# Kernel optimization log

Hardware: AMD Instinct MI355X
Metric: run time of the kernel (lower is better)

## Reference

```python
import jax, jax.numpy as jnp
import numpy as np

_T = lambda a: jnp.swapaxes(a, -1, -2)
EPS_TRI = 0.01   # block_tridiagonal_solve epsilon
EPS_CHOL = 0.01  # block_cholesky epsilon
EPS_BS = 1e-4    # batch_block_cholesky_solve epsilon


def _forward(z_samples, A_base, b_base, Q_sqrt, ms, Ri_sqrts, noise):
    n, T, K = z_samples.shape
    D = A_base.shape[-1]
    I = jnp.eye(D, dtype=z_samples.dtype)

    # ---- AQbFunction on z_samples[:, :-1]
    zt = z_samples[:, :-1]                                    # [n,T-1,K]
    As = jnp.einsum('ntk,kij->ntij', zt, A_base)              # [n,T-1,D,D]
    bs = jnp.einsum('ntk,kd->ntd', zt, b_base)                # [n,T-1,D]
    Qi_sqrts = jnp.einsum('ntk,kij->ntij', zt, Q_sqrt)        # [n,T-1,D,D]

    # ---- convert_lds_to_block_tridiag
    Qis = Qi_sqrts @ _T(Qi_sqrts)                             # [n,T-1,D,D]
    Ris = Ri_sqrts @ _T(Ri_sqrts)                             # [T,D,D]
    Jl = -jnp.einsum('ntij,ntjk->ntik', Qis, As)              # [n,T-1,D,D]
    pad_t = lambda a, w: jnp.pad(a, ((0, 0), w) + ((0, 0),) * (a.ndim - 2))
    Jd = (pad_t(-jnp.einsum('ntji,ntjk->ntik', As, Jl), (0, 1))
          + pad_t(Qis, (1, 0)) + Ris[None])                   # [n,T,D,D]
    h = (pad_t(jnp.einsum('ntij,ntj->nti', Jl, bs), (0, 1))
         + pad_t(jnp.einsum('ntij,ntj->nti', Qis, bs), (1, 0))
         + jnp.einsum('tij,tj->ti', Ris, ms)[None])           # [n,T,D]

    # time-major for scans
    Jd_t = jnp.swapaxes(Jd, 0, 1)    # [T,n,D,D]
    Jl_t = jnp.swapaxes(Jl, 0, 1)    # [T-1,n,D,D]
    h_t = jnp.swapaxes(h, 0, 1)      # [T,n,D]

    # ---- block_tridiagonal_solve (Thomas-style forward elim + back subst)
    J0 = Jd_t[0] + EPS_TRI * I
    c0 = _T(jnp.linalg.solve(J0, _T(Jl_t[0])))
    d0 = jnp.linalg.solve(J0, h_t[0][..., None])[..., 0]
    Jl_pad = jnp.concatenate([Jl_t, jnp.zeros_like(Jl_t[:1])], 0)  # [T,n,D,D]

    def fwd_step(carry, x):
        c_prev, d_prev = carry
        Jd_k, Jl_prev, Jl_cur, h_k = x
        Jk = Jd_k - Jl_prev @ c_prev + EPS_TRI * I
        c_k = _T(jnp.linalg.solve(Jk, _T(Jl_cur)))
        rhs = h_k - (Jl_prev @ d_prev[..., None])[..., 0]
        d_k = jnp.linalg.solve(Jk, rhs[..., None])[..., 0]
        return (c_k, d_k), (c_k, d_k)

    _, (cs, ds) = jax.lax.scan(fwd_step, (c0, d0),
                               (Jd_t[1:], Jl_t, Jl_pad[1:], h_t[1:]))
    d_all = jnp.concatenate([d0[None], ds], 0)   # [T,n,D]
    c_all = jnp.concatenate([c0[None], cs[:-1]], 0)  # [T-1,n,D,D]

    def bwd_step(x_next, inp):
        d_k, c_k = inp
        x_k = d_k - (c_k @ x_next[..., None])[..., 0]
        return x_k, x_k

    _, xs = jax.lax.scan(bwd_step, d_all[-1], (d_all[:-1], c_all), reverse=True)
    mu = jnp.swapaxes(jnp.concatenate([xs, d_all[-1:]], 0), 0, 1)  # [n,T,D]

    # ---- block_cholesky
    L0 = jnp.linalg.cholesky(Jd_t[0] + EPS_CHOL * I)

    def chol_step(L_prev, x):
        Jd_k, Jl_k = x
        Ll = _T(jnp.linalg.solve(_T(L_prev), _T(Jl_k)))
        L_k = jnp.linalg.cholesky(Jd_k - Ll @ _T(Ll) + EPS_CHOL * I)
        return L_k, (L_k, Ll)

    _, (Ls, Lls) = jax.lax.scan(chol_step, L0, (Jd_t[1:], Jl_t))
    L_all = jnp.concatenate([L0[None], Ls], 0)   # [T,n,D,D]

    # ---- batch_block_cholesky_solve (forward substitution on regularized L^T)
    Lr = L_all + EPS_BS * I
    z_t = jnp.swapaxes(noise.reshape(n, T, D), 0, 1)  # [T,n,D]
    x0 = jnp.linalg.solve(_T(Lr[0]), z_t[0][..., None])[..., 0]

    def samp_step(x_prev, inp):
        L_k, Ll_prev, zk = inp
        rhs = zk - (_T(Ll_prev) @ x_prev[..., None])[..., 0]
        x_k = jnp.linalg.solve(_T(L_k), rhs[..., None])[..., 0]
        return x_k, x_k

    _, xs2 = jax.lax.scan(samp_step, x0, (Lr[1:], Lls, z_t[1:]))
    x = jnp.swapaxes(jnp.concatenate([x0[None], xs2], 0), 0, 1)  # [n,T,D]
    return x + mu


def setup_inputs() -> dict:
    key = jax.random.key(0)
    k = jax.random.split(key, 7)
    n, T, D, K = 64, 256, 32, 8
    dt = jnp.float32
    I = jnp.eye(D, dtype=dt)
    z_samples = jax.random.normal(k[0], (n, T, K), dt)
    noise = jax.random.normal(k[1], (n, T * D), dt)
    # params per LDSVariational/AQbFunction init (+ tiny jitter to avoid degeneracy)
    A_base = 0.8 * jnp.tile(I, (K, 1, 1)) + 0.01 * jax.random.normal(k[2], (K, D, D), dt)
    b_base = 0.01 * jax.random.normal(k[3], (K, D), dt)
    Q_sqrt = jnp.tile(I, (K, 1, 1)) + 0.01 * jax.random.normal(k[4], (K, D, D), dt)
    ms = 0.1 * jax.random.normal(k[5], (T, D), dt)
    Ri_sqrts = 10.0 * jnp.tile(I, (T, 1, 1)) + 0.01 * jax.random.normal(k[6], (T, D, D), dt)  # 1/sqrt(0.01)=10
    return {"z_samples": z_samples, "A_base": A_base, "b_base": b_base,
            "Q_sqrt": Q_sqrt, "ms": ms, "Ri_sqrts": Ri_sqrts, "noise": noise}


def reference(z_samples, A_base, b_base, Q_sqrt, ms, Ri_sqrts, noise):
    return _forward(z_samples, A_base, b_base, Q_sqrt, ms, Ri_sqrts, noise)
```

## Files before the change

### kernel.cpp

```cpp
#include <hip/hip_runtime.h>
#include <cstddef>

#define LD 33
#define IDX(r,c) ((r)*LD+(c))
#define EPS_TRI 0.01f
#define EPS_BS 1e-4f
#define F4C(v,e) ((e)==0?(v).x:(e)==1?(v).y:(e)==2?(v).z:(v).w)
#define WAVE_FENCE() __builtin_amdgcn_wave_barrier()

#define NCH0 14
#define CSZ0 19
#define NCH1 18
#define CSZ1 15
#define WARM 6


__device__ __forceinline__ float4 xor1(const float4 v) {
  float4 r;
  r.x = __shfl_xor(v.x, 1);
  r.y = __shfl_xor(v.y, 1);
  r.z = __shfl_xor(v.z, 1);
  r.w = __shfl_xor(v.w, 1);
  return r;
}

__global__ __launch_bounds__(256) void ris_kernel(const float* __restrict__ Ri,
                                                  const float* __restrict__ ms,
                                                  float* __restrict__ Ris,
                                                  float* __restrict__ Rm) {
  const int t = blockIdx.x;
  const int tid = threadIdx.x;
  __shared__ float sR[32*LD];
  __shared__ float sRis[32*LD];
  __shared__ float sm[32];
  {
    const int e = tid * 4;
    const int r = e >> 5, c = e & 31;
    const float4 v = *(const float4*)(Ri + (size_t)t*1024 + e);
    sR[IDX(r,c)+0] = v.x; sR[IDX(r,c)+1] = v.y; sR[IDX(r,c)+2] = v.z; sR[IDX(r,c)+3] = v.w;
    if (tid < 32) sm[tid] = ms[t*32 + tid];
  }
  __syncthreads();
  const int r = tid >> 3, c0 = (tid & 7) * 4;
  float a0=0.f,a1=0.f,a2=0.f,a3=0.f;
#pragma unroll
  for (int p = 0; p < 32; p++) {
    const float rr = sR[IDX(r,p)];
    a0 += rr * sR[IDX(c0+0,p)];
    a1 += rr * sR[IDX(c0+1,p)];
    a2 += rr * sR[IDX(c0+2,p)];
    a3 += rr * sR[IDX(c0+3,p)];
  }
  sRis[IDX(r,c0+0)] = a0; sRis[IDX(r,c0+1)] = a1;
  sRis[IDX(r,c0+2)] = a2; sRis[IDX(r,c0+3)] = a3;
  float4 o; o.x=a0; o.y=a1; o.z=a2; o.w=a3;
  *(float4*)(Ris + (size_t)t*1024 + r*32 + c0) = o;
  __syncthreads();
  if (tid < 32) {
    float acc = 0.f;
#pragma unroll
    for (int j = 0; j < 32; j++) acc += sRis[IDX(tid,j)] * sm[j];
    Rm[t*32 + tid] = acc;
  }
}

__global__ __launch_bounds__(256) void pre_kernel(
    const float* __restrict__ z, const float* __restrict__ A_base,
    const float* __restrict__ b_base, const float* __restrict__ Q_sqrt,
    const float* __restrict__ Ris, const float* __restrict__ Rm,
    float* __restrict__ Jdb, float* __restrict__ Pm, float* __restrict__ h_ws) {
  const int n = blockIdx.x >> 8;
  const int t = blockIdx.x & 255;
  const int tid = threadIdx.x;
  const int r = tid >> 3, c0 = (tid & 7) * 4;
  const bool hcv = (t < 255);
  const bool hpv = (t >= 1);
  __shared__ __align__(16) float sAs[32*LD], sQs[32*LD], sQsp[32*LD];
  __shared__ __align__(16) float sQis[32*LD], sQisp[32*LD], sP[32*LD];
  __shared__ float s_z[16];
  __shared__ float s_bs[32], s_bsp[32];
  if (tid < 8)       s_z[tid] = hcv ? z[((size_t)n << 11) + t*8 + tid] : 0.f;
  else if (tid < 16) s_z[tid] = hpv ? z[((size_t)n << 11) + (t-1)*8 + (tid-8)] : 0.f;
  __syncthreads();
  {
    float a0=0,a1=0,a2=0,a3=0,q0=0,q1=0,q2=0,q3=0,p0=0,p1=0,p2=0,p3=0;
#pragma unroll
    for (int kq = 0; kq < 8; kq++) {
      const float zc = s_z[kq], zp = s_z[8+kq];
      const float4 av = *(const float4*)(A_base + kq*1024 + r*32 + c0);
      const float4 qv = *(const float4*)(Q_sqrt + kq*1024 + r*32 + c0);
      a0 += zc*av.x; a1 += zc*av.y; a2 += zc*av.z; a3 += zc*av.w;
      q0 += zc*qv.x; q1 += zc*qv.y; q2 += zc*qv.z; q3 += zc*qv.w;
      p0 += zp*qv.x; p1 += zp*qv.y; p2 += zp*qv.z; p3 += zp*qv.w;
    }
    sAs[IDX(r,c0+0)]=a0; sAs[IDX(r,c0+1)]=a1; sAs[IDX(r,c0+2)]=a2; sAs[IDX(r,c0+3)]=a3;
    sQs[IDX(r,c0+0)]=q0; sQs[IDX(r,c0+1)]=q1; sQs[IDX(r,c0+2)]=q2; sQs[IDX(r,c0+3)]=q3;
    sQsp[IDX(r,c0+0)]=p0; sQsp[IDX(r,c0+1)]=p1; sQsp[IDX(r,c0+2)]=p2; sQsp[IDX(r,c0+3)]=p3;
    if (tid < 32) {
      float b = 0.f;
#pragma unroll
      for (int kq = 0; kq < 8; kq++) b += s_z[kq] * b_base[kq*32 + tid];
      s_bs[tid] = b;
    } else if (tid < 64) {
      const int i = tid - 32;
      float b = 0.f;
#pragma unroll
      for (int kq = 0; kq < 8; kq++) b += s_z[8+kq] * b_base[kq*32 + i];
      s_bsp[i] = b;
    }
  }
  __syncthreads();
  {
    float a0=0,a1=0,a2=0,a3=0,b0=0,b1=0,b2=0,b3=0;
#pragma unroll
    for (int p = 0; p < 32; p++) {
      const float qr = sQs[IDX(r,p)];
      a0 += qr * sQs[IDX(c0+0,p)];
      a1 += qr * sQs[IDX(c0+1,p)];
      a2 += qr * sQs[IDX(c0+2,p)];
      a3 += qr * sQs[IDX(c0+3,p)];
      const float pr2 = sQsp[IDX(r,p)];
      b0 += pr2 * sQsp[IDX(c0+0,p)];
      b1 += pr2 * sQsp[IDX(c0+1,p)];
      b2 += pr2 * sQsp[IDX(c0+2,p)];
      b3 += pr2 * sQsp[IDX(c0+3,p)];
    }
    sQis[IDX(r,c0+0)]=a0; sQis[IDX(r,c0+1)]=a1; sQis[IDX(r,c0+2)]=a2; sQis[IDX(r,c0+3)]=a3;
    sQisp[IDX(r,c0+0)]=b0; sQisp[IDX(r,c0+1)]=b1; sQisp[IDX(r,c0+2)]=b2; sQisp[IDX(r,c0+3)]=b3;
  }
  __syncthreads();
  {
    float a0=0,a1=0,a2=0,a3=0;
#pragma unroll
    for (int p = 0; p < 32; p++) {
      const float qr = sQis[IDX(r,p)];
      a0 += qr * sAs[IDX(p,c0+0)];
      a1 += qr * sAs[IDX(p,c0+1)];
      a2 += qr * sAs[IDX(p,c0+2)];
      a3 += qr * sAs[IDX(p,c0+3)];
    }
    sP[IDX(r,c0+0)]=a0; sP[IDX(r,c0+1)]=a1; sP[IDX(r,c0+2)]=a2; sP[IDX(r,c0+3)]=a3;
    if (hcv) {
      float4 v; v.x=a0; v.y=a1; v.z=a2; v.w=a3;
      *(float4*)(Pm + ((size_t)(n*255 + t))*1024 + r*32 + c0) = v;
    }
  }
  __syncthreads();
  {
    const float4 rv = *(const float4*)(Ris + (size_t)t*1024 + r*32 + c0);
    float j0 = rv.x, j1 = rv.y, j2 = rv.z, j3 = rv.w;
    if (r == c0+0) j0 += EPS_TRI;
    else if (r == c0+1) j1 += EPS_TRI;
    else if (r == c0+2) j2 += EPS_TRI;
    else if (r == c0+3) j3 += EPS_TRI;
    if (hcv) {
#pragma unroll
      for (int p = 0; p < 32; p++) {
        const float ar = sAs[IDX(p,r)];
        j0 += ar * sP[IDX(p,c0+0)];
        j1 += ar * sP[IDX(p,c0+1)];
        j2 += ar * sP[IDX(p,c0+2)];
        j3 += ar * sP[IDX(p,c0+3)];
      }
    }
    if (hpv) {
      j0 += sQisp[IDX(r,c0+0)];
      j1 += sQisp[IDX(r,c0+1)];
      j2 += sQisp[IDX(r,c0+2)];
      j3 += sQisp[IDX(r,c0+3)];
    }
    float4 v; v.x=j0; v.y=j1; v.z=j2; v.w=j3;
    *(float4*)(Jdb + ((size_t)(n*256 + t))*1024 + r*32 + c0) = v;
    if (tid < 32) {
      float h = Rm[t*32 + tid];
      if (hcv) {
        float a = 0.f;
#pragma unroll
        for (int j = 0; j < 32; j++) a += sP[IDX(tid,j)] * s_bs[j];
        h -= a;
      }
      if (hpv) {
        float a = 0.f;
#pragma unroll
        for (int j = 0; j < 32; j++) a += sQisp[IDX(tid,j)] * s_bsp[j];
        h += a;
      }
      h_ws[((size_t)(n*256 + t))*32 + tid] = h;
    }
  }
}

union __align__(16) ChainShared {
  struct {
    float sCT[32*36];
    float sB[32*36];
    float sPiv[64];
    float s_rhs[32], s_d[32], s_invp[32];
  } r0;
  struct {
    float sLl[32*36];
    float sLT[32*36];
    float sLrow[32*36];
    float sCol[32];
    float s_x[32], s_invd[32], s_invr[32];
  } r1;
};

__global__ __launch_bounds__(64) void chain_kernel(
    const float* __restrict__ Jdb, const float* __restrict__ Pm,
    const float* __restrict__ h_ws, const float* __restrict__ noise,
    float* __restrict__ c_ws, float* __restrict__ d_ws, float* __restrict__ x_ws) {
  const int bid  = blockIdx.x;
  const int role = (bid >= 64*NCH0) ? 1 : 0;
  const int rem  = bid - role*64*NCH0;
  const int bn   = rem & 63;
  const int ch   = rem >> 6;
  const int lane = threadIdx.x;
  const int r    = lane >> 1;
  const int h2   = lane & 1;
  const int c16  = h2 * 16;

  const int csz       = role ? CSZ1 : CSZ0;
  const int k_out     = ch * csz;
  const int k_start   = (ch == 0) ? 0 : (k_out - WARM);
  const int k_end_raw = k_out + csz;
  const int k_end     = (k_end_raw > 256) ? 256 : k_end_raw;

  const float* Jb = Jdb + (size_t)bn * 256 * 1024;
  const float* Pb = Pm  + (size_t)bn * 255 * 1024;

  __shared__ ChainShared su;

  if (role == 0) {
    float* sCT = su.r0.sCT;
    float* sB  = su.r0.sB;
    float* sPiv = su.r0.sPiv;
    float* s_rhs = su.r0.s_rhs;
    float* s_d   = su.r0.s_d;
    float* s_invp = su.r0.s_invp;
    const float* hb = h_ws + (size_t)bn * 256 * 32;

    const int offO = c16;
    const int offX = 16 - c16;

    float jrow[16]; float4 pq[4]; float hq;
    {
      float4 j4[4];
#pragma unroll
      for (int q = 0; q < 4; q++) j4[q] = *(const float4*)(Jb + (size_t)k_start*1024 + r*32 + c16 + 4*q);
#pragma unroll
      for (int q = 0; q < 4; q++) pq[q] = *(const float4*)(Pb + (size_t)k_start*1024 + r*32 + c16 + 4*q);
      hq = hb[k_start*32 + r];
#pragma unroll
      for (int i = 0; i < 16; i++) jrow[i] = F4C(j4[i >> 2], i & 3);
    }

    for (int k = k_start; k < k_end; k++) {
      float4 jn4[4], pn[4]; float hn = 0.f;
      if (k + 1 < 256) {
#pragma unroll
        for (int q = 0; q < 4; q++)
          jn4[q] = *(const float4*)(Jb + (size_t)(k+1)*1024 + r*32 + c16 + 4*q);
        hn = hb[(k+1)*32 + r];
        if (k + 1 < 255) {
#pragma unroll
          for (int q = 0; q < 4; q++)
            pn[q] = *(const float4*)(Pb + (size_t)(k+1)*1024 + r*32 + c16 + 4*q);
        }
      }
      if (h2 == 0) s_rhs[r] = hq;
      float g[32];
      if (h2 == 1) {
#pragma unroll
        for (int i = 0; i < 32; i++) g[i] = (i == r) ? 1.f : 0.f;
      }
#pragma unroll
      for (int i = 0; i < 16; i++) {
        const float oth = __shfl_xor(jrow[i], 1);
        if (h2 == 0) { g[i] = jrow[i]; g[16+i] = oth; }
      }
      if (r == 0) {
#pragma unroll
        for (int q = 0; q < 8; q++) {
          float4 v; v.x=g[4*q]; v.y=g[4*q+1]; v.z=g[4*q+2]; v.w=g[4*q+3];
          *(float4*)(&sPiv[h2*32 + 4*q]) = v;
        }
      }
      WAVE_FENCE();
      float my_piv = 1.f;
#pragma unroll
      for (int j = 0; j < 32; j++) {
        const float pj_own = sPiv[h2*32 + j];
        const float pj_oth = __shfl_xor(pj_own, 1);
        const float dpiv = h2 ? pj_oth : pj_own;
        const float ip = __builtin_amdgcn_rcpf(dpiv);
        const float gj_own = g[j];
        const float gj_oth = __shfl_xor(gj_own, 1);
        float f = (h2 ? gj_oth : gj_own) * ip;
        if (j == r) { my_piv = dpiv; f = 0.f; }
#pragma unroll
        for (int q = 0; q < 8; q++) {
          const float4 v = *(const float4*)(&sPiv[h2*32 + 4*q]);
          g[4*q+0] -= f * v.x;
          g[4*q+1] -= f * v.y;
          g[4*q+2] -= f * v.z;
          g[4*q+3] -= f * v.w;
        }
        if (j + 1 < 32) {
          WAVE_FENCE();
          if (r == j + 1) {
#pragma unroll
            for (int q = 0; q < 8; q++) {
              float4 v; v.x=g[4*q]; v.y=g[4*q+1]; v.z=g[4*q+2]; v.w=g[4*q+3];
              *(float4*)(&sPiv[h2*32 + 4*q]) = v;
            }
          }
          WAVE_FENCE();
        }
      }
      const float ipv = __builtin_amdgcn_rcpf(my_piv);
      if (h2 == 0) s_invp[r] = ipv;
      else {
        const int s7 = r & 7;
#pragma unroll
        for (int q = 0; q < 8; q++) {
          float4 v; v.x=g[4*q]; v.y=g[4*q+1]; v.z=g[4*q+2]; v.w=g[4*q+3];
          *(float4*)(&sB[r*36 + 4*(q ^ s7)]) = v;
        }
      }
      WAVE_FENCE();
      if (h2 == 1) {
        float acc = 0.f;
#pragma unroll
        for (int q = 0; q < 8; q++) {
          const float4 rv = *(const float4*)(&s_rhs[4*q]);
          acc += g[4*q]*rv.x + g[4*q+1]*rv.y + g[4*q+2]*rv.z + g[4*q+3]*rv.w;
        }
        const float dv = acc * ipv;
        s_d[r] = dv;
        if (k >= k_out) d_ws[((size_t)(bn*256 + k))*32 + r] = dv;
      }
      float4 poK[4];
      if (k < 255) {
#pragma unroll
        for (int q = 0; q < 4; q++) poK[q] = xor1(pq[q]);
        float outv[16];
#pragma unroll
        for (int i = 0; i < 16; i++) {
          const int c = c16 + i;
          const float* bb = &sB[c*36];
          const int s7 = c & 7;
          float acc = 0.f;
#pragma unroll
          for (int q = 0; q < 4; q++) {
            const float4 v0 = *(const float4*)(bb + 4*((4*h2 + q) ^ s7));
            acc += pq[q].x*v0.x + pq[q].y*v0.y + pq[q].z*v0.z + pq[q].w*v0.w;
            const float4 v1 = *(const float4*)(bb + 4*(((4 - 4*h2) + q) ^ s7));
            acc += poK[q].x*v1.x + poK[q].y*v1.y + poK[q].z*v1.z + poK[q].w*v1.w;
          }
          outv[i] = -acc * s_invp[c];
        }
        if (k >= k_out) {
#pragma unroll
          for (int q = 0; q < 4; q++) {
            float4 v; v.x=outv[4*q]; v.y=outv[4*q+1]; v.z=outv[4*q+2]; v.w=outv[4*q+3];
            *(float4*)(c_ws + ((size_t)(bn*255 + k))*1024 + r*32 + c16 + 4*q) = v;
          }
        }
#pragma unroll
        for (int i = 0; i < 16; i++) sCT[(c16+i)*36 + r] = outv[i];
      }
      WAVE_FENCE();
      if (k + 1 < k_end) {
        float a_own = 0.f;
#pragma unroll
        for (int q = 0; q < 4; q++) {
          const float4 dv = *(const float4*)(&s_d[c16 + 4*q]);
          a_own += pq[q].x*dv.x + pq[q].y*dv.y + pq[q].z*dv.z + pq[q].w*dv.w;
        }
        hq = hn + a_own + __shfl_xor(a_own, 1);
#pragma unroll
        for (int i = 0; i < 16; i++) {
          const float* base = &sCT[(c16 + i) * 36];
          float acc = F4C(jn4[i >> 2], i & 3);
#pragma unroll
          for (int q = 0; q < 4; q++) {
            const float4 v0 = *(const float4*)(base + offO + 4*q);
            acc += pq[q].x*v0.x + pq[q].y*v0.y + pq[q].z*v0.z + pq[q].w*v0.w;
            const float4 v1 = *(const float4*)(base + offX + 4*q);
            acc += poK[q].x*v1.x + poK[q].y*v1.y + poK[q].z*v1.z + poK[q].w*v1.w;
          }
          jrow[i] = acc;
        }
#pragma unroll
        for (int q = 0; q < 4; q++) pq[q] = pn[q];
      }
    }
  } else {
    float* sLl   = su.r1.sLl;
    float* sLT   = su.r1.sLT;
    float* sLrow = su.r1.sLrow;
    float* sCol  = su.r1.sCol;
    float* s_x   = su.r1.s_x;
    float* s_invd = su.r1.s_invd;
    float* s_invr = su.r1.s_invr;
    const float* nb = noise + (size_t)bn * 8192;

    float mrow[16]; float4 pq[4]; float xr;
    {
      float4 j4[4];
#pragma unroll
      for (int q = 0; q < 4; q++) j4[q] = *(const float4*)(Jb + (size_t)k_start*1024 + r*32 + c16 + 4*q);
#pragma unroll
      for (int q = 0; q < 4; q++) pq[q] = *(const float4*)(Pb + (size_t)k_start*1024 + r*32 + c16 + 4*q);
      xr = nb[k_start*32 + r];
#pragma unroll
      for (int i = 0; i < 16; i++) mrow[i] = F4C(j4[i >> 2], i & 3);
    }

    for (int k = k_start; k < k_end; k++) {
      float4 jn4[4], pn[4]; float nn = 0.f;
      if (k + 1 < 256) {
#pragma unroll
        for (int q = 0; q < 4; q++)
          jn4[q] = *(const float4*)(Jb + (size_t)(k+1)*1024 + r*32 + c16 + 4*q);
        nn = nb[(k+1)*32 + r];
        if (k + 1 < 255) {
#pragma unroll
          for (int q = 0; q < 4; q++)
            pn[q] = *(const float4*)(Pb + (size_t)(k+1)*1024 + r*32 + c16 + 4*q);
        }
      }
#pragma unroll
      for (int j = 0; j < 32; j++) {
        const int jl = j & 15, jh = j >> 4;
        WAVE_FENCE();
        if (h2 == jh) sCol[r] = mrow[jl];
        WAVE_FENCE();
        const float dpiv = sCol[j];
        const float fr   = sCol[r];
        const float sq = sqrtf(dpiv);
        const float inv = __builtin_amdgcn_rcpf(sq);
        if (h2 == 0 && r >= j) {
          const float lv = (r == j) ? sq : fr*inv;
          sLT[36*j + 4*((r>>2) ^ (j&7)) + (r&3)] = lv;
          sLrow[36*r + 4*((j>>2) ^ (r&7)) + (j&3)] = lv;
        }
        if (lane == 0) { s_invd[j] = inv; s_invr[j] = __builtin_amdgcn_rcpf(sq + EPS_BS); }
        const float s2 = (r > j) ? fr*inv*inv : 0.f;
#pragma unroll
        for (int q = 0; q < 4; q++) {
          const float4 cc = *(const float4*)(&sCol[c16 + 4*q]);
          mrow[4*q+0] -= s2 * cc.x;
          mrow[4*q+1] -= s2 * cc.y;
          mrow[4*q+2] -= s2 * cc.z;
          mrow[4*q+3] -= s2 * cc.w;
        }
      }
      WAVE_FENCE();
      float sv[16];
      if (k < 255) {
#pragma unroll
        for (int q = 0; q < 4; q++) {
          sv[4*q+0] = -pq[q].x; sv[4*q+1] = -pq[q].y;
          sv[4*q+2] = -pq[q].z; sv[4*q+3] = -pq[q].w;
        }
#pragma unroll
        for (int j = 31; j >= 0; j--) {
          const int jl = j & 15, jh = j >> 4;
          const float invdj = s_invd[j];
          const float v = sv[jl] * invdj;
          const float w = __shfl_xor(v, 1);
          const float xj = (h2 == jh) ? v : w;
          if (h2 == jh) sv[jl] = v;
#pragma unroll
          for (int q = 0; q < 4; q++) {
            if (4*q < j) {
              const float4 lv = *(const float4*)(&sLrow[36*j + 4*(((h2<<2)+q) ^ (j&7))]);
#pragma unroll
              for (int e = 0; e < 4; e++) {
                const int iLo = 4*q+e, iHi = 16+4*q+e;
                const float le = F4C(lv, e);
                if (iHi < j) {
                  sv[4*q+e] -= le * xj;
                } else if (iLo < j) {
                  const float m = (h2 == 0) ? le : 0.f;
                  sv[4*q+e] -= m * xj;
                }
              }
            }
          }
        }
        const int s7r = r & 7;
#pragma unroll
        for (int q = 0; q < 4; q++) {
          float4 v4; v4.x=sv[4*q]; v4.y=sv[4*q+1]; v4.z=sv[4*q+2]; v4.w=sv[4*q+3];
          *(float4*)(&sLl[36*r + 4*(((h2<<2)+q) ^ s7r)]) = v4;
        }
      }
      WAVE_FENCE();
      if (k + 1 < k_end) {
        float lrow[32];
#pragma unroll
        for (int gi = 0; gi < 16; gi++) {
          const float o = __shfl_xor(sv[gi], 1);
          lrow[gi]      = h2 ? o : sv[gi];
          lrow[16 + gi] = h2 ? sv[gi] : o;
        }
#pragma unroll
        for (int i = 0; i < 16; i++) {
          const int c = c16 + i;
          const int s7c = c & 7;
          float acc = 0.f;
#pragma unroll
          for (int q = 0; q < 8; q++) {
            const float4 v4 = *(const float4*)(&sLl[36*c + 4*(q ^ s7c)]);
            acc += lrow[4*q]*v4.x + lrow[4*q+1]*v4.y + lrow[4*q+2]*v4.z + lrow[4*q+3]*v4.w;
          }
          mrow[i] = F4C(jn4[i >> 2], i & 3) - acc;
        }
      }
      {
        float lc[32];
        const int s7r = r & 7;
#pragma unroll
        for (int q = 0; q < 8; q++) {
          const float4 v = *(const float4*)(&sLT[36*r + 4*(q ^ s7r)]);
          lc[4*q]=v.x; lc[4*q+1]=v.y; lc[4*q+2]=v.z; lc[4*q+3]=v.w;
        }
        float xp = xr;
        float myx = 0.f;
#pragma unroll
        for (int j = 31; j >= 0; j--) {
          const float xj = __shfl(xp * s_invr[j], 2*j);
          if (j == r) myx = xj;
          if (r < j) xp -= lc[j] * xj;
        }
        if (h2 == 0) {
          s_x[r] = myx;
          if (k >= k_out) x_ws[((size_t)(bn*256 + k))*32 + r] = myx;
        }
      }
      WAVE_FENCE();
      if (k + 1 < k_end) {
        float a_own = 0.f;
        const int rg = r >> 2, re = r & 3;
#pragma unroll
        for (int jj = 0; jj < 16; jj++)
          a_own += sLl[36*(c16+jj) + 4*(rg ^ (jj & 7)) + re] * s_x[c16+jj];
        xr = nn - (a_own + __shfl_xor(a_own, 1));
#pragma unroll
        for (int q = 0; q < 4; q++) pq[q] = pn[q];
      }
    }
  }
}

__global__ __launch_bounds__(64) void bwd_kernel(const float* __restrict__ c_ws,
                                                 const float* __restrict__ d_ws,
                                                 const float* __restrict__ x_ws,
                                                 float* __restrict__ out) {
  const int bn = blockIdx.x >> 4;
  const int q  = blockIdx.x & 15;
  const int lane = threadIdx.x;
  const int r = lane >> 1, h2 = lane & 1, c16 = h2 * 16;
  const int k_lo = q * 16;
  const int k_seed = (q == 15) ? 255 : (k_lo + 23);
  __shared__ float s_mu[32];
  if (h2 == 0) {
    const float mu = d_ws[((size_t)(bn*256 + k_seed))*32 + r];
    s_mu[r] = mu;
    if (k_seed == 255)
      out[((size_t)(bn*256 + 255))*32 + r] = x_ws[((size_t)(bn*256 + 255))*32 + r] + mu;
  }
  WAVE_FENCE();
  for (int k = k_seed - 1; k >= k_lo; k--) {
    const float* cp = c_ws + ((size_t)(bn*255 + k))*1024 + r*32 + c16;
    const float4 v0 = *(const float4*)(cp + 0);
    const float4 v1 = *(const float4*)(cp + 4);
    const float4 v2 = *(const float4*)(cp + 8);
    const float4 v3 = *(const float4*)(cp + 12);
    float part = v0.x*s_mu[c16+0] + v0.y*s_mu[c16+1] + v0.z*s_mu[c16+2] + v0.w*s_mu[c16+3]
               + v1.x*s_mu[c16+4] + v1.y*s_mu[c16+5] + v1.z*s_mu[c16+6] + v1.w*s_mu[c16+7]
               + v2.x*s_mu[c16+8] + v2.y*s_mu[c16+9] + v2.z*s_mu[c16+10]+ v2.w*s_mu[c16+11]
               + v3.x*s_mu[c16+12]+ v3.y*s_mu[c16+13]+ v3.z*s_mu[c16+14]+ v3.w*s_mu[c16+15];
    part += __shfl_xor(part, 1);
    float mu = 0.f, xv = 0.f;
    if (h2 == 0) {
      mu = d_ws[((size_t)(bn*256 + k))*32 + r] - part;
      xv = x_ws[((size_t)(bn*256 + k))*32 + r];
    }
    WAVE_FENCE();
    if (h2 == 0) {
      s_mu[r] = mu;
      if (k < k_lo + 16) out[((size_t)(bn*256 + k))*32 + r] = xv + mu;
    }
    WAVE_FENCE();
  }
}

extern "C" void kernel_launch(void* const* d_in, const int* in_sizes, int n_in,
                              void* d_out, int out_size, void* d_ws, size_t ws_size,
                              hipStream_t stream) {
  const float* z      = (const float*)d_in[0];
  const float* A_base = (const float*)d_in[1];
  const float* b_base = (const float*)d_in[2];
  const float* Q_sqrt = (const float*)d_in[3];
  const float* ms     = (const float*)d_in[4];
  const float* Ri     = (const float*)d_in[5];
  const float* noise  = (const float*)d_in[6];
  float* out = (float*)d_out;

  float* ws = (float*)d_ws;
  const size_t SZ_C = (size_t)64*255*1024;
  const size_t SZ_J = (size_t)64*256*1024;
  const size_t SZ_V = (size_t)64*256*32;

  float* c_ws  = ws;
  float* Jdb   = c_ws + SZ_C;
  float* Pm    = Jdb + SZ_J;
  float* hbuf  = Pm + SZ_C;
  float* d_vec = hbuf + SZ_V;
  float* x_vec = d_vec + SZ_V;
  float* Ris   = x_vec + SZ_V;
  float* Rm    = Ris + (size_t)256*1024;

  ris_kernel<<<256, 256, 0, stream>>>(Ri, ms, Ris, Rm);
  pre_kernel<<<16384, 256, 0, stream>>>(z, A_base, b_base, Q_sqrt, Ris, Rm, Jdb, Pm, hbuf);
  chain_kernel<<<64*(NCH0+NCH1), 64, 0, stream>>>(Jdb, Pm, hbuf, noise, c_ws, d_vec, x_vec);
  bwd_kernel<<<1024, 64, 0, stream>>>(c_ws, d_vec, x_vec, out);
}
```

Measured before the change: 1.029 ms.

## Split chain kernel into separate solve and Cholesky kernels with finer chunks

Replaces the single role-dispatched chain kernel with two kernels, one for the block-tridiagonal forward elimination and one for the Cholesky sampling chain. Each kernel uses 32 chunks of 8 steps with a 6-step warm-up, so more independent blocks run at once and the sequential chain per block is shorter. The elimination loop is also restructured: the Schur update and the rhs update now happen at the top of each step, and the XOR-swizzled shared layouts are replaced by plain rows. In exchange, the warm-up steps are a larger share of total work, there is an extra launch, and the two roles no longer overlap within one grid.

```diff
diff --git a/kernel.cpp b/kernel.cpp
--- a/kernel.cpp
+++ b/kernel.cpp
@@ -8,12 +8,9 @@
 #define F4C(v,e) ((e)==0?(v).x:(e)==1?(v).y:(e)==2?(v).z:(v).w)
 #define WAVE_FENCE() __builtin_amdgcn_wave_barrier()
 
-#define NCH0 14
-#define CSZ0 19
-#define NCH1 18
-#define CSZ1 15
+#define NCH 32
+#define CSZ 8
 #define WARM 6
-
 
 __device__ __forceinline__ float4 xor1(const float4 v) {
   float4 r;
@@ -190,368 +187,383 @@
   }
 }
 
-union __align__(16) ChainShared {
-  struct {
-    float sCT[32*36];
-    float sB[32*36];
-    float sPiv[64];
-    float s_rhs[32], s_d[32], s_invp[32];
-  } r0;
-  struct {
-    float sLl[32*36];
-    float sLT[32*36];
-    float sLrow[32*36];
-    float sCol[32];
-    float s_x[32], s_invd[32], s_invr[32];
-  } r1;
-};
-
-__global__ __launch_bounds__(64) void chain_kernel(
+__global__ __launch_bounds__(64) void chain0_kernel(
     const float* __restrict__ Jdb, const float* __restrict__ Pm,
-    const float* __restrict__ h_ws, const float* __restrict__ noise,
-    float* __restrict__ c_ws, float* __restrict__ d_ws, float* __restrict__ x_ws) {
-  const int bid  = blockIdx.x;
-  const int role = (bid >= 64*NCH0) ? 1 : 0;
-  const int rem  = bid - role*64*NCH0;
-  const int bn   = rem & 63;
-  const int ch   = rem >> 6;
+    const float* __restrict__ h_ws,
+    float* __restrict__ c_ws, float* __restrict__ d_ws) {
+  const int bn   = blockIdx.x & 63;
+  const int ch   = blockIdx.x >> 6;
   const int lane = threadIdx.x;
   const int r    = lane >> 1;
   const int h2   = lane & 1;
   const int c16  = h2 * 16;
 
-  const int csz       = role ? CSZ1 : CSZ0;
-  const int k_out     = ch * csz;
+  const int k_out     = ch * CSZ;
   const int k_start   = (ch == 0) ? 0 : (k_out - WARM);
-  const int k_end_raw = k_out + csz;
+  const int k_end_raw = k_out + CSZ;
   const int k_end     = (k_end_raw > 256) ? 256 : k_end_raw;
+  const int vec_start = k_start;
 
   const float* Jb = Jdb + (size_t)bn * 256 * 1024;
   const float* Pb = Pm  + (size_t)bn * 255 * 1024;
-
-  __shared__ ChainShared su;
-
-  if (role == 0) {
-    float* sCT = su.r0.sCT;
-    float* sB  = su.r0.sB;
-    float* sPiv = su.r0.sPiv;
-    float* s_rhs = su.r0.s_rhs;
-    float* s_d   = su.r0.s_d;
-    float* s_invp = su.r0.s_invp;
-    const float* hb = h_ws + (size_t)bn * 256 * 32;
-
-    const int offO = c16;
-    const int offX = 16 - c16;
-
-    float jrow[16]; float4 pq[4]; float hq;
+  const float* hb = h_ws + (size_t)bn * 256 * 32;
+
+  __shared__ float sCT[32*36];
+  __shared__ float sB[32*36];
+  __shared__ float sPiv[64];
+  __shared__ float s_rhs[32], s_d[32], s_invp[32];
+
+  float4 jq[4], pq[4], pq_prev[4]; float hq;
+#pragma unroll
+  for (int q = 0; q < 4; q++) jq[q] = *(const float4*)(Jb + (size_t)k_start*1024 + r*32 + c16 + 4*q);
+#pragma unroll
+  for (int q = 0; q < 4; q++) pq[q] = *(const float4*)(Pb + (size_t)k_start*1024 + r*32 + c16 + 4*q);
+#pragma unroll
+  for (int q = 0; q < 4; q++) pq_prev[q] = pq[q];
+  hq = hb[k_start*32 + r];
+
+  for (int k = k_start; k < k_end; k++) {
+    float4 jn[4], pn[4]; float hn = 0.f;
+    if (k + 1 < 256) {
+#pragma unroll
+      for (int q = 0; q < 4; q++)
+        jn[q] = *(const float4*)(Jb + (size_t)(k+1)*1024 + r*32 + c16 + 4*q);
+      hn = hb[(k+1)*32 + r];
+      if (k + 1 < 255) {
+#pragma unroll
+        for (int q = 0; q < 4; q++)
+          pn[q] = *(const float4*)(Pb + (size_t)(k+1)*1024 + r*32 + c16 + 4*q);
+      }
+    }
+    float prA[16], prB[16];
     {
-      float4 j4[4];
-#pragma unroll
-      for (int q = 0; q < 4; q++) j4[q] = *(const float4*)(Jb + (size_t)k_start*1024 + r*32 + c16 + 4*q);
-#pragma unroll
-      for (int q = 0; q < 4; q++) pq[q] = *(const float4*)(Pb + (size_t)k_start*1024 + r*32 + c16 + 4*q);
-      hq = hb[k_start*32 + r];
-#pragma unroll
-      for (int i = 0; i < 16; i++) jrow[i] = F4C(j4[i >> 2], i & 3);
-    }
-
-    for (int k = k_start; k < k_end; k++) {
-      float4 jn4[4], pn[4]; float hn = 0.f;
-      if (k + 1 < 256) {
-#pragma unroll
-        for (int q = 0; q < 4; q++)
-          jn4[q] = *(const float4*)(Jb + (size_t)(k+1)*1024 + r*32 + c16 + 4*q);
-        hn = hb[(k+1)*32 + r];
-        if (k + 1 < 255) {
-#pragma unroll
-          for (int q = 0; q < 4; q++)
-            pn[q] = *(const float4*)(Pb + (size_t)(k+1)*1024 + r*32 + c16 + 4*q);
-        }
-      }
-      if (h2 == 0) s_rhs[r] = hq;
-      float g[32];
-      if (h2 == 1) {
-#pragma unroll
-        for (int i = 0; i < 32; i++) g[i] = (i == r) ? 1.f : 0.f;
-      }
+      float own[16], oth[16];
+#pragma unroll
+      for (int i = 0; i < 16; i++) own[i] = F4C(pq_prev[i >> 2], i & 3);
+#pragma unroll
+      for (int i = 0; i < 16; i++) oth[i] = __shfl_xor(own[i], 1);
 #pragma unroll
       for (int i = 0; i < 16; i++) {
-        const float oth = __shfl_xor(jrow[i], 1);
-        if (h2 == 0) { g[i] = jrow[i]; g[16+i] = oth; }
-      }
-      if (r == 0) {
-#pragma unroll
-        for (int q = 0; q < 8; q++) {
-          float4 v; v.x=g[4*q]; v.y=g[4*q+1]; v.z=g[4*q+2]; v.w=g[4*q+3];
-          *(float4*)(&sPiv[h2*32 + 4*q]) = v;
-        }
-      }
-      WAVE_FENCE();
-      float my_piv = 1.f;
-#pragma unroll
-      for (int j = 0; j < 32; j++) {
-        const float pj_own = sPiv[h2*32 + j];
-        const float pj_oth = __shfl_xor(pj_own, 1);
-        const float dpiv = h2 ? pj_oth : pj_own;
-        const float ip = __builtin_amdgcn_rcpf(dpiv);
-        const float gj_own = g[j];
-        const float gj_oth = __shfl_xor(gj_own, 1);
-        float f = (h2 ? gj_oth : gj_own) * ip;
-        if (j == r) { my_piv = dpiv; f = 0.f; }
-#pragma unroll
-        for (int q = 0; q < 8; q++) {
-          const float4 v = *(const float4*)(&sPiv[h2*32 + 4*q]);
-          g[4*q+0] -= f * v.x;
-          g[4*q+1] -= f * v.y;
-          g[4*q+2] -= f * v.z;
-          g[4*q+3] -= f * v.w;
-        }
-        if (j + 1 < 32) {
-          WAVE_FENCE();
-          if (r == j + 1) {
-#pragma unroll
-            for (int q = 0; q < 8; q++) {
-              float4 v; v.x=g[4*q]; v.y=g[4*q+1]; v.z=g[4*q+2]; v.w=g[4*q+3];
-              *(float4*)(&sPiv[h2*32 + 4*q]) = v;
-            }
-          }
-          WAVE_FENCE();
-        }
-      }
-      const float ipv = __builtin_amdgcn_rcpf(my_piv);
-      if (h2 == 0) s_invp[r] = ipv;
-      else {
-        const int s7 = r & 7;
-#pragma unroll
-        for (int q = 0; q < 8; q++) {
-          float4 v; v.x=g[4*q]; v.y=g[4*q+1]; v.z=g[4*q+2]; v.w=g[4*q+3];
-          *(float4*)(&sB[r*36 + 4*(q ^ s7)]) = v;
-        }
-      }
-      WAVE_FENCE();
-      if (h2 == 1) {
-        float acc = 0.f;
-#pragma unroll
-        for (int q = 0; q < 8; q++) {
-          const float4 rv = *(const float4*)(&s_rhs[4*q]);
-          acc += g[4*q]*rv.x + g[4*q+1]*rv.y + g[4*q+2]*rv.z + g[4*q+3]*rv.w;
-        }
-        const float dv = acc * ipv;
-        s_d[r] = dv;
-        if (k >= k_out) d_ws[((size_t)(bn*256 + k))*32 + r] = dv;
-      }
-      float4 poK[4];
-      if (k < 255) {
-#pragma unroll
-        for (int q = 0; q < 4; q++) poK[q] = xor1(pq[q]);
-        float outv[16];
-#pragma unroll
-        for (int i = 0; i < 16; i++) {
-          const int c = c16 + i;
-          const float* bb = &sB[c*36];
-          const int s7 = c & 7;
-          float acc = 0.f;
-#pragma unroll
-          for (int q = 0; q < 4; q++) {
-            const float4 v0 = *(const float4*)(bb + 4*((4*h2 + q) ^ s7));
-            acc += pq[q].x*v0.x + pq[q].y*v0.y + pq[q].z*v0.z + pq[q].w*v0.w;
-            const float4 v1 = *(const float4*)(bb + 4*(((4 - 4*h2) + q) ^ s7));
-            acc += poK[q].x*v1.x + poK[q].y*v1.y + poK[q].z*v1.z + poK[q].w*v1.w;
-          }
-          outv[i] = -acc * s_invp[c];
-        }
-        if (k >= k_out) {
-#pragma unroll
-          for (int q = 0; q < 4; q++) {
-            float4 v; v.x=outv[4*q]; v.y=outv[4*q+1]; v.z=outv[4*q+2]; v.w=outv[4*q+3];
-            *(float4*)(c_ws + ((size_t)(bn*255 + k))*1024 + r*32 + c16 + 4*q) = v;
-          }
-        }
-#pragma unroll
-        for (int i = 0; i < 16; i++) sCT[(c16+i)*36 + r] = outv[i];
-      }
-      WAVE_FENCE();
-      if (k + 1 < k_end) {
+        prA[i] = h2 ? oth[i] : own[i];
+        prB[i] = h2 ? own[i] : oth[i];
+      }
+    }
+    if (k >= vec_start) {
+      float rhs_r = hq;
+      if (k > vec_start) {
         float a_own = 0.f;
 #pragma unroll
         for (int q = 0; q < 4; q++) {
           const float4 dv = *(const float4*)(&s_d[c16 + 4*q]);
-          a_own += pq[q].x*dv.x + pq[q].y*dv.y + pq[q].z*dv.z + pq[q].w*dv.w;
-        }
-        hq = hn + a_own + __shfl_xor(a_own, 1);
+          a_own += pq_prev[q].x*dv.x + pq_prev[q].y*dv.y + pq_prev[q].z*dv.z + pq_prev[q].w*dv.w;
+        }
+        rhs_r += a_own + __shfl_xor(a_own, 1);
+      }
+      if (h2 == 0) s_rhs[r] = rhs_r;
+    }
+    float tmp[16];
+#pragma unroll
+    for (int i = 0; i < 16; i++) tmp[i] = F4C(jq[i >> 2], i & 3);
+    if (k > k_start) {
+#pragma unroll
+      for (int i = 0; i < 16; i++) {
+        const int c = c16 + i;
+        float acc = 0.f;
+#pragma unroll
+        for (int q = 0; q < 4; q++) {
+          const float4 v0 = *(const float4*)(&sCT[c*36 + 4*q]);
+          acc += prA[4*q]*v0.x + prA[4*q+1]*v0.y + prA[4*q+2]*v0.z + prA[4*q+3]*v0.w;
+          const float4 v1 = *(const float4*)(&sCT[c*36 + 16 + 4*q]);
+          acc += prB[4*q]*v1.x + prB[4*q+1]*v1.y + prB[4*q+2]*v1.z + prB[4*q+3]*v1.w;
+        }
+        tmp[i] += acc;
+      }
+    }
+    float g[32];
+    if (h2 == 1) {
+#pragma unroll
+      for (int i = 0; i < 32; i++) g[i] = (i == r) ? 1.f : 0.f;
+    }
+#pragma unroll
+    for (int i = 0; i < 16; i++) {
+      const float oth = __shfl_xor(tmp[i], 1);
+      if (h2 == 0) { g[i] = tmp[i]; g[16+i] = oth; }
+    }
+    if (r == 0) {
+#pragma unroll
+      for (int q = 0; q < 8; q++) {
+        float4 v; v.x=g[4*q]; v.y=g[4*q+1]; v.z=g[4*q+2]; v.w=g[4*q+3];
+        *(float4*)(&sPiv[h2*32 + 4*q]) = v;
+      }
+    }
+    WAVE_FENCE();
+    float my_piv = 1.f;
+#pragma unroll
+    for (int j = 0; j < 32; j++) {
+      float pr_[32];
+#pragma unroll
+      for (int q = 0; q < 8; q++) {
+        const float4 v = *(const float4*)(&sPiv[h2*32 + 4*q]);
+        pr_[4*q]=v.x; pr_[4*q+1]=v.y; pr_[4*q+2]=v.z; pr_[4*q+3]=v.w;
+      }
+      const float dj_own = pr_[j];
+      const float dj_oth = __shfl_xor(dj_own, 1);
+      const float dpiv = h2 ? dj_oth : dj_own;
+      const float ip = __builtin_amdgcn_rcpf(dpiv);
+      const float gj_own = g[j];
+      const float gj_oth = __shfl_xor(gj_own, 1);
+      float f = (h2 ? gj_oth : gj_own) * ip;
+      if (j == r) { my_piv = dpiv; f = 0.f; }
+#pragma unroll
+      for (int i = 0; i < 32; i++) g[i] -= f * pr_[i];
+      if (j + 1 < 32) {
+        WAVE_FENCE();
+        if (r == j + 1) {
+#pragma unroll
+          for (int q = 0; q < 8; q++) {
+            float4 v; v.x=g[4*q]; v.y=g[4*q+1]; v.z=g[4*q+2]; v.w=g[4*q+3];
+            *(float4*)(&sPiv[h2*32 + 4*q]) = v;
+          }
+        }
+        WAVE_FENCE();
+      }
+    }
+    const float ipv = __builtin_amdgcn_rcpf(my_piv);
+    if (h2 == 0) s_invp[r] = ipv;
+    else {
+#pragma unroll
+      for (int q = 0; q < 8; q++) {
+        float4 v; v.x=g[4*q]; v.y=g[4*q+1]; v.z=g[4*q+2]; v.w=g[4*q+3];
+        *(float4*)(&sB[r*36 + 4*q]) = v;
+      }
+    }
+    WAVE_FENCE();
+    if (h2 == 1 && k >= vec_start) {
+      float acc = 0.f;
+#pragma unroll
+      for (int q = 0; q < 8; q++) {
+        const float4 rv = *(const float4*)(&s_rhs[4*q]);
+        acc += g[4*q]*rv.x + g[4*q+1]*rv.y + g[4*q+2]*rv.z + g[4*q+3]*rv.w;
+      }
+      const float dv = acc * ipv;
+      s_d[r] = dv;
+      if (k >= k_out) d_ws[((size_t)(bn*256 + k))*32 + r] = dv;
+    }
+    if (k < 255) {
+      float pcA[16], pcB[16];
+      {
+        float own[16], oth[16];
+#pragma unroll
+        for (int i = 0; i < 16; i++) own[i] = F4C(pq[i >> 2], i & 3);
+#pragma unroll
+        for (int i = 0; i < 16; i++) oth[i] = __shfl_xor(own[i], 1);
 #pragma unroll
         for (int i = 0; i < 16; i++) {
-          const float* base = &sCT[(c16 + i) * 36];
-          float acc = F4C(jn4[i >> 2], i & 3);
-#pragma unroll
-          for (int q = 0; q < 4; q++) {
-            const float4 v0 = *(const float4*)(base + offO + 4*q);
-            acc += pq[q].x*v0.x + pq[q].y*v0.y + pq[q].z*v0.z + pq[q].w*v0.w;
-            const float4 v1 = *(const float4*)(base + offX + 4*q);
-            acc += poK[q].x*v1.x + poK[q].y*v1.y + poK[q].z*v1.z + poK[q].w*v1.w;
-          }
-          jrow[i] = acc;
-        }
-#pragma unroll
-        for (int q = 0; q < 4; q++) pq[q] = pn[q];
-      }
-    }
-  } else {
-    float* sLl   = su.r1.sLl;
-    float* sLT   = su.r1.sLT;
-    float* sLrow = su.r1.sLrow;
-    float* sCol  = su.r1.sCol;
-    float* s_x   = su.r1.s_x;
-    float* s_invd = su.r1.s_invd;
-    float* s_invr = su.r1.s_invr;
-    const float* nb = noise + (size_t)bn * 8192;
-
-    float mrow[16]; float4 pq[4]; float xr;
-    {
-      float4 j4[4];
-#pragma unroll
-      for (int q = 0; q < 4; q++) j4[q] = *(const float4*)(Jb + (size_t)k_start*1024 + r*32 + c16 + 4*q);
-#pragma unroll
-      for (int q = 0; q < 4; q++) pq[q] = *(const float4*)(Pb + (size_t)k_start*1024 + r*32 + c16 + 4*q);
-      xr = nb[k_start*32 + r];
-#pragma unroll
-      for (int i = 0; i < 16; i++) mrow[i] = F4C(j4[i >> 2], i & 3);
-    }
-
-    for (int k = k_start; k < k_end; k++) {
-      float4 jn4[4], pn[4]; float nn = 0.f;
-      if (k + 1 < 256) {
+          pcA[i] = h2 ? oth[i] : own[i];
+          pcB[i] = h2 ? own[i] : oth[i];
+        }
+      }
+      float outv[16];
+#pragma unroll
+      for (int i = 0; i < 16; i++) {
+        const int c = c16 + i;
+        float acc = 0.f;
+#pragma unroll
+        for (int q = 0; q < 4; q++) {
+          const float4 v0 = *(const float4*)(&sB[c*36 + 4*q]);
+          acc += pcA[4*q]*v0.x + pcA[4*q+1]*v0.y + pcA[4*q+2]*v0.z + pcA[4*q+3]*v0.w;
+          const float4 v1 = *(const float4*)(&sB[c*36 + 16 + 4*q]);
+          acc += pcB[4*q]*v1.x + pcB[4*q+1]*v1.y + pcB[4*q+2]*v1.z + pcB[4*q+3]*v1.w;
+        }
+        outv[i] = -acc * s_invp[c];
+      }
+      if (k >= k_out) {
+#pragma unroll
+        for (int q = 0; q < 4; q++) {
+          float4 v; v.x=outv[4*q]; v.y=outv[4*q+1]; v.z=outv[4*q+2]; v.w=outv[4*q+3];
+          *(float4*)(c_ws + ((size_t)(bn*255 + k))*1024 + r*32 + c16 + 4*q) = v;
+        }
+      }
+#pragma unroll
+      for (int i = 0; i < 16; i++) sCT[(c16+i)*36 + r] = outv[i];
+    }
+    WAVE_FENCE();
+#pragma unroll
+    for (int q = 0; q < 4; q++) { jq[q] = jn[q]; pq_prev[q] = pq[q]; pq[q] = pn[q]; }
+    hq = hn;
+  }
+}
+
+__global__ __launch_bounds__(64) void chain1_kernel(
+    const float* __restrict__ Jdb, const float* __restrict__ Pm,
+    const float* __restrict__ noise, float* __restrict__ x_ws) {
+  const int bn   = blockIdx.x & 63;
+  const int ch   = blockIdx.x >> 6;
+  const int lane = threadIdx.x;
+  const int r    = lane >> 1;
+  const int h2   = lane & 1;
+  const int c16  = h2 * 16;
+
+  const int k_out     = ch * CSZ;
+  const int k_start   = (ch == 0) ? 0 : (k_out - WARM);
+  const int k_end_raw = k_out + CSZ;
+  const int k_end     = (k_end_raw > 256) ? 256 : k_end_raw;
+
+  const float* Jb = Jdb + (size_t)bn * 256 * 1024;
+  const float* Pb = Pm  + (size_t)bn * 255 * 1024;
+  const float* nb = noise + (size_t)bn * 8192;
+
+  __shared__ float sLl[32*36];
+  __shared__ float sLT[32*36];
+  __shared__ float sLrow[32*36];
+  __shared__ float sCol[32];
+  __shared__ float s_x[32], s_invd[32], s_invr[32];
+
+  float mrow[16]; float4 pq[4]; float xr;
+  {
+    float4 j4[4];
+#pragma unroll
+    for (int q = 0; q < 4; q++) j4[q] = *(const float4*)(Jb + (size_t)k_start*1024 + r*32 + c16 + 4*q);
+#pragma unroll
+    for (int q = 0; q < 4; q++) pq[q] = *(const float4*)(Pb + (size_t)k_start*1024 + r*32 + c16 + 4*q);
+    xr = nb[k_start*32 + r];
+#pragma unroll
+    for (int i = 0; i < 16; i++) mrow[i] = F4C(j4[i >> 2], i & 3);
+  }
+
+  for (int k = k_start; k < k_end; k++) {
+    float4 jn4[4], pn[4]; float nn = 0.f;
+    if (k + 1 < 256) {
+#pragma unroll
+      for (int q = 0; q < 4; q++)
+        jn4[q] = *(const float4*)(Jb + (size_t)(k+1)*1024 + r*32 + c16 + 4*q);
+      nn = nb[(k+1)*32 + r];
+      if (k + 1 < 255) {
 #pragma unroll
         for (int q = 0; q < 4; q++)
-          jn4[q] = *(const float4*)(Jb + (size_t)(k+1)*1024 + r*32 + c16 + 4*q);
-        nn = nb[(k+1)*32 + r];
-        if (k + 1 < 255) {
-#pragma unroll
-          for (int q = 0; q < 4; q++)
-            pn[q] = *(const float4*)(Pb + (size_t)(k+1)*1024 + r*32 + c16 + 4*q);
-        }
-      }
-#pragma unroll
-      for (int j = 0; j < 32; j++) {
+          pn[q] = *(const float4*)(Pb + (size_t)(k+1)*1024 + r*32 + c16 + 4*q);
+      }
+    }
+#pragma unroll
+    for (int j = 0; j < 32; j++) {
+      const int jl = j & 15, jh = j >> 4;
+      WAVE_FENCE();
+      if (h2 == jh) sCol[r] = mrow[jl];
+      WAVE_FENCE();
+      const float dpiv = sCol[j];
+      const float fr   = sCol[r];
+      const float sq = sqrtf(dpiv);
+      const float inv = __builtin_amdgcn_rcpf(sq);
+      if (h2 == 0 && r >= j) {
+        const float lv = (r == j) ? sq : fr*inv;
+        sLT[36*j + 4*((r>>2) ^ (j&7)) + (r&3)] = lv;
+        sLrow[36*r + 4*((j>>2) ^ (r&7)) + (j&3)] = lv;
+      }
+      if (lane == 0) { s_invd[j] = inv; s_invr[j] = __builtin_amdgcn_rcpf(sq + EPS_BS); }
+      const float s2 = (r > j) ? fr*inv*inv : 0.f;
+#pragma unroll
+      for (int q = 0; q < 4; q++) {
+        const float4 cc = *(const float4*)(&sCol[c16 + 4*q]);
+        mrow[4*q+0] -= s2 * cc.x;
+        mrow[4*q+1] -= s2 * cc.y;
+        mrow[4*q+2] -= s2 * cc.z;
+        mrow[4*q+3] -= s2 * cc.w;
+      }
+    }
+    WAVE_FENCE();
+    float sv[16];
+    if (k < 255) {
+#pragma unroll
+      for (int q = 0; q < 4; q++) {
+        sv[4*q+0] = -pq[q].x; sv[4*q+1] = -pq[q].y;
+        sv[4*q+2] = -pq[q].z; sv[4*q+3] = -pq[q].w;
+      }
+#pragma unroll
+      for (int j = 31; j >= 0; j--) {
         const int jl = j & 15, jh = j >> 4;
-        WAVE_FENCE();
-        if (h2 == jh) sCol[r] = mrow[jl];
-        WAVE_FENCE();
-        const float dpiv = sCol[j];
-        const float fr   = sCol[r];
-        const float sq = sqrtf(dpiv);
-        const float inv = __builtin_amdgcn_rcpf(sq);
-        if (h2 == 0 && r >= j) {
-          const float lv = (r == j) ? sq : fr*inv;
-          sLT[36*j + 4*((r>>2) ^ (j&7)) + (r&3)] = lv;
-          sLrow[36*r + 4*((j>>2) ^ (r&7)) + (j&3)] = lv;
-        }
-        if (lane == 0) { s_invd[j] = inv; s_invr[j] = __builtin_amdgcn_rcpf(sq + EPS_BS); }
-        const float s2 = (r > j) ? fr*inv*inv : 0.f;
+        const float invdj = s_invd[j];
+        const float v = sv[jl] * invdj;
+        const float w = __shfl_xor(v, 1);
+        const float xj = (h2 == jh) ? v : w;
+        if (h2 == jh) sv[jl] = v;
 #pragma unroll
         for (int q = 0; q < 4; q++) {
-          const float4 cc = *(const float4*)(&sCol[c16 + 4*q]);
-          mrow[4*q+0] -= s2 * cc.x;
-          mrow[4*q+1] -= s2 * cc.y;
-          mrow[4*q+2] -= s2 * cc.z;
-          mrow[4*q+3] -= s2 * cc.w;
-        }
-      }
-      WAVE_FENCE();
-      float sv[16];
-      if (k < 255) {
-#pragma unroll
-        for (int q = 0; q < 4; q++) {
-          sv[4*q+0] = -pq[q].x; sv[4*q+1] = -pq[q].y;
-          sv[4*q+2] = -pq[q].z; sv[4*q+3] = -pq[q].w;
-        }
-#pragma unroll
-        for (int j = 31; j >= 0; j--) {
-          const int jl = j & 15, jh = j >> 4;
-          const float invdj = s_invd[j];
-          const float v = sv[jl] * invdj;
-          const float w = __shfl_xor(v, 1);
-          const float xj = (h2 == jh) ? v : w;
-          if (h2 == jh) sv[jl] = v;
-#pragma unroll
-          for (int q = 0; q < 4; q++) {
-            if (4*q < j) {
-              const float4 lv = *(const float4*)(&sLrow[36*j + 4*(((h2<<2)+q) ^ (j&7))]);
-#pragma unroll
-              for (int e = 0; e < 4; e++) {
-                const int iLo = 4*q+e, iHi = 16+4*q+e;
-                const float le = F4C(lv, e);
-                if (iHi < j) {
-                  sv[4*q+e] -= le * xj;
-                } else if (iLo < j) {
-                  const float m = (h2 == 0) ? le : 0.f;
-                  sv[4*q+e] -= m * xj;
-                }
+          if (4*q < j) {
+            const float4 lv = *(const float4*)(&sLrow[36*j + 4*(((h2<<2)+q) ^ (j&7))]);
+#pragma unroll
+            for (int e = 0; e < 4; e++) {
+              const int iLo = 4*q+e, iHi = 16+4*q+e;
+              const float le = F4C(lv, e);
+              if (iHi < j) {
+                sv[4*q+e] -= le * xj;
+              } else if (iLo < j) {
+                const float m = (h2 == 0) ? le : 0.f;
+                sv[4*q+e] -= m * xj;
               }
             }
           }
         }
-        const int s7r = r & 7;
-#pragma unroll
-        for (int q = 0; q < 4; q++) {
-          float4 v4; v4.x=sv[4*q]; v4.y=sv[4*q+1]; v4.z=sv[4*q+2]; v4.w=sv[4*q+3];
-          *(float4*)(&sLl[36*r + 4*(((h2<<2)+q) ^ s7r)]) = v4;
-        }
-      }
-      WAVE_FENCE();
-      if (k + 1 < k_end) {
-        float lrow[32];
-#pragma unroll
-        for (int gi = 0; gi < 16; gi++) {
-          const float o = __shfl_xor(sv[gi], 1);
-          lrow[gi]      = h2 ? o : sv[gi];
-          lrow[16 + gi] = h2 ? sv[gi] : o;
-        }
-#pragma unroll
-        for (int i = 0; i < 16; i++) {
-          const int c = c16 + i;
-          const int s7c = c & 7;
-          float acc = 0.f;
-#pragma unroll
-          for (int q = 0; q < 8; q++) {
-            const float4 v4 = *(const float4*)(&sLl[36*c + 4*(q ^ s7c)]);
-            acc += lrow[4*q]*v4.x + lrow[4*q+1]*v4.y + lrow[4*q+2]*v4.z + lrow[4*q+3]*v4.w;
-          }
-          mrow[i] = F4C(jn4[i >> 2], i & 3) - acc;
-        }
-      }
-      {
-        float lc[32];
-        const int s7r = r & 7;
+      }
+      const int s7r = r & 7;
+#pragma unroll
+      for (int q = 0; q < 4; q++) {
+        float4 v4; v4.x=sv[4*q]; v4.y=sv[4*q+1]; v4.z=sv[4*q+2]; v4.w=sv[4*q+3];
+        *(float4*)(&sLl[36*r + 4*(((h2<<2)+q) ^ s7r)]) = v4;
+      }
+    }
+    WAVE_FENCE();
+    if (k + 1 < k_end) {
+      float lrow[32];
+#pragma unroll
+      for (int gi = 0; gi < 16; gi++) {
+        const float o = __shfl_xor(sv[gi], 1);
+        lrow[gi]      = h2 ? o : sv[gi];
+        lrow[16 + gi] = h2 ? sv[gi] : o;
+      }
+#pragma unroll
+      for (int i = 0; i < 16; i++) {
+        const int c = c16 + i;
+        const int s7c = c & 7;
+        float acc = 0.f;
 #pragma unroll
         for (int q = 0; q < 8; q++) {
-          const float4 v = *(const float4*)(&sLT[36*r + 4*(q ^ s7r)]);
-          lc[4*q]=v.x; lc[4*q+1]=v.y; lc[4*q+2]=v.z; lc[4*q+3]=v.w;
-        }
-        float xp = xr;
-        float myx = 0.f;
-#pragma unroll
-        for (int j = 31; j >= 0; j--) {
-          const float xj = __shfl(xp * s_invr[j], 2*j);
-          if (j == r) myx = xj;
-          if (r < j) xp -= lc[j] * xj;
-        }
-        if (h2 == 0) {
-          s_x[r] = myx;
-          if (k >= k_out) x_ws[((size_t)(bn*256 + k))*32 + r] = myx;
-        }
-      }
-      WAVE_FENCE();
-      if (k + 1 < k_end) {
-        float a_own = 0.f;
-        const int rg = r >> 2, re = r & 3;
-#pragma unroll
-        for (int jj = 0; jj < 16; jj++)
-          a_own += sLl[36*(c16+jj) + 4*(rg ^ (jj & 7)) + re] * s_x[c16+jj];
-        xr = nn - (a_own + __shfl_xor(a_own, 1));
-#pragma unroll
-        for (int q = 0; q < 4; q++) pq[q] = pn[q];
-      }
+          const float4 v4 = *(const float4*)(&sLl[36*c + 4*(q ^ s7c)]);
+          acc += lrow[4*q]*v4.x + lrow[4*q+1]*v4.y + lrow[4*q+2]*v4.z + lrow[4*q+3]*v4.w;
+        }
+        mrow[i] = F4C(jn4[i >> 2], i & 3) - acc;
+      }
+    }
+    {
+      float lc[32];
+      const int s7r = r & 7;
+#pragma unroll
+      for (int q = 0; q < 8; q++) {
+        const float4 v = *(const float4*)(&sLT[36*r + 4*(q ^ s7r)]);
+        lc[4*q]=v.x; lc[4*q+1]=v.y; lc[4*q+2]=v.z; lc[4*q+3]=v.w;
+      }
+      float xp = xr;
+      float myx = 0.f;
+#pragma unroll
+      for (int j = 31; j >= 0; j--) {
+        const float xj = __shfl(xp * s_invr[j], 2*j);
+        if (j == r) myx = xj;
+        if (r < j) xp -= lc[j] * xj;
+      }
+      if (h2 == 0) {
+        s_x[r] = myx;
+        if (k >= k_out) x_ws[((size_t)(bn*256 + k))*32 + r] = myx;
+      }
+    }
+    WAVE_FENCE();
+    if (k + 1 < k_end) {
+      float a_own = 0.f;
+      const int rg = r >> 2, re = r & 3;
+#pragma unroll
+      for (int jj = 0; jj < 16; jj++)
+        a_own += sLl[36*(c16+jj) + 4*(rg ^ (jj & 7)) + re] * s_x[c16+jj];
+      xr = nn - (a_own + __shfl_xor(a_own, 1));
+#pragma unroll
+      for (int q = 0; q < 4; q++) pq[q] = pn[q];
     }
   }
 }
@@ -627,6 +639,7 @@
 
   ris_kernel<<<256, 256, 0, stream>>>(Ri, ms, Ris, Rm);
   pre_kernel<<<16384, 256, 0, stream>>>(z, A_base, b_base, Q_sqrt, Ris, Rm, Jdb, Pm, hbuf);
-  chain_kernel<<<64*(NCH0+NCH1), 64, 0, stream>>>(Jdb, Pm, hbuf, noise, c_ws, d_vec, x_vec);
+  chain0_kernel<<<64*NCH, 64, 0, stream>>>(Jdb, Pm, hbuf, c_ws, d_vec);
+  chain1_kernel<<<64*NCH, 64, 0, stream>>>(Jdb, Pm, noise, x_vec);
   bwd_kernel<<<1024, 64, 0, stream>>>(c_ws, d_vec, x_vec, out);
 }
```

Result: slower. 1.260 ms (+22.4%).
